# Optimization experiments

Hardware: AMD Instinct MI355X
Metric: run time of the kernel (lower is better)

Reference implementation:

```python
import jax, jax.numpy as jnp
import numpy as np

B, S, D = 4, 4096, 64


def setup_inputs() -> dict:
    key = jax.random.key(0)
    ks = jax.random.split(key, 11)
    std = 1.0 / np.sqrt(D)
    inp = {
        "q": jax.random.normal(ks[0], (B, S, D), jnp.float32),
        "k": jax.random.normal(ks[1], (B, S, D), jnp.float32),
        "v": jax.random.normal(ks[2], (B, S, D), jnp.float32),
        # torch.nn.Linear params: weight [out,in], bias [out]
        "Wq": jax.random.uniform(ks[3], (D, D), jnp.float32, -std, std),
        "bq": jax.random.uniform(ks[4], (D,), jnp.float32, -std, std),
        "Wk": jax.random.uniform(ks[5], (D, D), jnp.float32, -std, std),
        "bk": jax.random.uniform(ks[6], (D,), jnp.float32, -std, std),
        "Wv": jax.random.uniform(ks[7], (D, D), jnp.float32, -std, std),
        "bv": jax.random.uniform(ks[8], (D,), jnp.float32, -std, std),
        "Wp": jax.random.uniform(ks[9], (D, D), jnp.float32, -std, std),
        "bp": jax.random.uniform(ks[10], (D,), jnp.float32, -std, std),
    }
    return inp


def reference(q, k, v, Wq, bq, Wk, bk, Wv, bv, Wp, bp):
    Q = q @ Wq.T + bq                      # [B,S,D]
    K = k @ Wk.T + bk
    V = v @ Wv.T + bv
    scale = 1.0 / jnp.sqrt(jnp.asarray(Q.shape[-1], Q.dtype))
    s = jnp.einsum('bqd,bkd->bqk', Q, K) * scale   # [B,S,S]
    # faithful to torch.tril(full_like(-inf), diagonal=-1): -inf strictly below diagonal
    i = jnp.arange(S)[:, None]
    j = jnp.arange(S)[None, :]
    s = jnp.where(i > j, -jnp.inf, s)
    o = jax.nn.softmax(s, axis=-1) @ V             # [B,S,D]
    return o @ Wp.T + bp
```

## Files before the change

### kernel.cpp

```cpp
#include <hip/hip_runtime.h>
#include <hip/hip_bf16.h>

#define S_LEN 4096
#define D_DIM 64
#define NBATCH 4

typedef unsigned short u16;
typedef unsigned int u32;
typedef __attribute__((ext_vector_type(8))) __bf16 bf16x8;
typedef __attribute__((ext_vector_type(4))) float f32x4;
typedef __attribute__((ext_vector_type(16))) float f32x16;

__device__ __forceinline__ u16 f_to_bf16u(float f) {
    union { float f; u32 u; } x; x.f = f;
    u32 r = x.u + 0x7fffu + ((x.u >> 16) & 1u);
    return (u16)(r >> 16);
}

__global__ __launch_bounds__(256, 2)
void proj_qkv_kernel(const float* __restrict__ q, const float* __restrict__ k,
                     const float* __restrict__ v,
                     const float* __restrict__ Wq, const float* __restrict__ bq,
                     const float* __restrict__ Wk, const float* __restrict__ bk,
                     const float* __restrict__ Wv, const float* __restrict__ bv,
                     u16* __restrict__ Qb, u16* __restrict__ Kb, u16* __restrict__ Vt)
{
    __shared__ __align__(16) u16 vt[64 * 72];

    const int p = blockIdx.y;
    const float* inp  = (p == 0) ? q  : (p == 1) ? k  : v;
    const float* W    = (p == 0) ? Wq : (p == 1) ? Wk : Wv;
    const float* bias = (p == 0) ? bq : (p == 1) ? bk : bv;
    const float scl   = (p == 0) ? 0.18033688011112042f : 1.0f;

    const int tid  = threadIdx.x;
    const int wid  = tid >> 6;
    const int lane = tid & 63;
    const int ln   = lane & 15;
    const int qd   = lane >> 4;
    const int row0 = blockIdx.x * 64;
    const int r0w  = row0 + wid * 16;

    bf16x8 afrag[2];
#pragma unroll
    for (int c = 0; c < 2; ++c) {
        const float* src = inp + (r0w + ln) * 64 + c * 32 + qd * 8;
        float4 f0 = *(const float4*)src;
        float4 f1 = *(const float4*)(src + 4);
        bf16x8 a;
        a[0] = (__bf16)f0.x; a[1] = (__bf16)f0.y; a[2] = (__bf16)f0.z; a[3] = (__bf16)f0.w;
        a[4] = (__bf16)f1.x; a[5] = (__bf16)f1.y; a[6] = (__bf16)f1.z; a[7] = (__bf16)f1.w;
        afrag[c] = a;
    }

    bf16x8 bfrag[4][2];
    float  bcol[4];
#pragma unroll
    for (int nb = 0; nb < 4; ++nb) {
        bcol[nb] = bias[nb * 16 + ln];
#pragma unroll
        for (int c = 0; c < 2; ++c) {
            const float* src = W + (nb * 16 + ln) * 64 + c * 32 + qd * 8;
            float4 f0 = *(const float4*)src;
            float4 f1 = *(const float4*)(src + 4);
            bf16x8 b;
            b[0] = (__bf16)f0.x; b[1] = (__bf16)f0.y; b[2] = (__bf16)f0.z; b[3] = (__bf16)f0.w;
            b[4] = (__bf16)f1.x; b[5] = (__bf16)f1.y; b[6] = (__bf16)f1.z; b[7] = (__bf16)f1.w;
            bfrag[nb][c] = b;
        }
    }

    f32x4 acc[4];
#pragma unroll
    for (int nb = 0; nb < 4; ++nb) acc[nb] = (f32x4){0.f, 0.f, 0.f, 0.f};
#pragma unroll
    for (int c = 0; c < 2; ++c)
#pragma unroll
        for (int nb = 0; nb < 4; ++nb)
            acc[nb] = __builtin_amdgcn_mfma_f32_16x16x32_bf16(afrag[c], bfrag[nb][c], acc[nb], 0, 0, 0);

    if (p < 2) {
        u16* dst = (p == 0) ? Qb : Kb;
#pragma unroll
        for (int nb = 0; nb < 4; ++nb)
#pragma unroll
            for (int r = 0; r < 4; ++r) {
                int row = r0w + qd * 4 + r;
                dst[row * 64 + nb * 16 + ln] = f_to_bf16u((acc[nb][r] + bcol[nb]) * scl);
            }
    } else {
#pragma unroll
        for (int nb = 0; nb < 4; ++nb)
#pragma unroll
            for (int r = 0; r < 4; ++r)
                vt[(wid * 16 + qd * 4 + r) * 72 + nb * 16 + ln] = f_to_bf16u(acc[nb][r] + bcol[nb]);
        __syncthreads();
        const int d  = tid >> 2;
        const int sc = tid & 3;
        const int b  = row0 >> 12;
        const int sb = row0 & 4095;
        __align__(16) u16 tmp[16];
#pragma unroll
        for (int i = 0; i < 16; ++i) tmp[i] = vt[(sc * 16 + i) * 72 + d];
        u16* dstp = Vt + (size_t)b * (64 * S_LEN) + d * S_LEN + sb + sc * 16;
        *(uint4*)(dstp)     = *(const uint4*)(tmp);
        *(uint4*)(dstp + 8) = *(const uint4*)(tmp + 8);
    }
}

__global__ __launch_bounds__(256, 2)
void flash_kernel(const u16* __restrict__ Qb, const u16* __restrict__ Kb,
                  const u16* __restrict__ Vt, u16* __restrict__ Op,
                  float* __restrict__ Lp)
{
    __shared__ __align__(16) u16 kv[2][2][64 * 64];
    __shared__ __align__(16) u16 pbuf[4][32 * 64];

    const int tid  = threadIdx.x;
    const int wid  = tid >> 6;
    const int lane = tid & 63;
    const int l31  = lane & 31;
    const int lh   = lane >> 5;
    const int sw7  = l31 & 7;

    const int bid   = blockIdx.x;
    const int half  = bid >> 8;
    const int idx   = bid & 255;
    const int batch = idx & 3;
    const int vv_   = idx >> 2;
    const int c     = vv_ & 3;
    const int rb16  = vv_ >> 2;
    const int rb    = half ? (31 - rb16) : rb16;
    const int first = 2 * rb;
    const int jt0   = first + ((c - first) & 3);
    const int i0w   = rb * 128 + wid * 32;

    const u16* qrow = Qb + ((size_t)batch * S_LEN + i0w + l31) * 64;
    bf16x8 qf[4];
#pragma unroll
    for (int c2 = 0; c2 < 4; ++c2)
        qf[c2] = *(const bf16x8*)(qrow + c2 * 16 + lh * 8);

    f32x16 o0, o1;
#pragma unroll
    for (int r = 0; r < 16; ++r) { o0[r] = 0.f; o1[r] = 0.f; }
    float lsum = 0.f;

    const int  srow = (tid & 127) >> 1;
    const int  sch0 = (tid & 1) * 4;
    const u16* kg   = Kb + ((size_t)batch * S_LEN + srow) * 64 + sch0 * 8;
    const u16* vg   = Vt + (size_t)batch * (64 * S_LEN) + srow * S_LEN + sch0 * 8;
    uint4 pf0, pf1, pf2, pf3;

    u16* pw = &pbuf[wid][0];
    int cur = 0;

    if (jt0 < 64) {
        {
            const int j0 = jt0 * 64;
            if (tid < 128) {
                const uint4* g = (const uint4*)(kg + (size_t)j0 * 64);
                pf0 = g[0]; pf1 = g[1]; pf2 = g[2]; pf3 = g[3];
            } else {
                const uint4* g = (const uint4*)(vg + j0);
                pf0 = g[0]; pf1 = g[1]; pf2 = g[2]; pf3 = g[3];
            }
            u16* base = &kv[0][(tid >> 7)][srow * 64];
            *(uint4*)(base + ((sch0 + 0) ^ (srow & 7)) * 8) = pf0;
            *(uint4*)(base + ((sch0 + 1) ^ (srow & 7)) * 8) = pf1;
            *(uint4*)(base + ((sch0 + 2) ^ (srow & 7)) * 8) = pf2;
            *(uint4*)(base + ((sch0 + 3) ^ (srow & 7)) * 8) = pf3;
        }

        for (int jt = jt0; jt < 64; jt += 4) {
            __syncthreads();
            const int j0   = jt * 64;
            const bool more = (jt + 4) < 64;
            if (more) {
                const int jn = (jt + 4) * 64;
                if (tid < 128) {
                    const uint4* g = (const uint4*)(kg + (size_t)jn * 64);
                    pf0 = g[0]; pf1 = g[1]; pf2 = g[2]; pf3 = g[3];
                } else {
                    const uint4* g = (const uint4*)(vg + jn);
                    pf0 = g[0]; pf1 = g[1]; pf2 = g[2]; pf3 = g[3];
                }
            }

            const u16* kb = &kv[cur][0][0];
            const u16* vb = &kv[cur][1][0];

            f32x16 s0, s1;
#pragma unroll
            for (int r = 0; r < 16; ++r) { s0[r] = 0.f; s1[r] = 0.f; }
#pragma unroll
            for (int c2 = 0; c2 < 4; ++c2) {
                const int ch = (2 * c2 + lh) ^ sw7;
                bf16x8 k0 = *(const bf16x8*)(kb + l31 * 64 + ch * 8);
                bf16x8 k1 = *(const bf16x8*)(kb + (32 + l31) * 64 + ch * 8);
                s0 = __builtin_amdgcn_mfma_f32_32x32x16_bf16(k0, qf[c2], s0, 0, 0, 0);
                s1 = __builtin_amdgcn_mfma_f32_32x32x16_bf16(k1, qf[c2], s1, 0, 0, 0);
            }

            const bool needmask = (j0 < i0w + 32);
            const int  qr = i0w + l31;
#pragma unroll
            for (int m = 0; m < 2; ++m) {
#pragma unroll
                for (int g = 0; g < 4; ++g) {
                    float p0, p1, p2, p3;
                    {
                        const f32x16& s = m ? s1 : s0;
                        p0 = exp2f(s[g * 4 + 0]);
                        p1 = exp2f(s[g * 4 + 1]);
                        p2 = exp2f(s[g * 4 + 2]);
                        p3 = exp2f(s[g * 4 + 3]);
                    }
                    if (needmask) {
                        const int kcol = j0 + m * 32 + 8 * g + 4 * lh;
                        p0 = (kcol + 0 < qr) ? 0.f : p0;
                        p1 = (kcol + 1 < qr) ? 0.f : p1;
                        p2 = (kcol + 2 < qr) ? 0.f : p2;
                        p3 = (kcol + 3 < qr) ? 0.f : p3;
                    }
                    lsum += (p0 + p1) + (p2 + p3);
                    u32 w0 = (u32)f_to_bf16u(p0) | ((u32)f_to_bf16u(p1) << 16);
                    u32 w1 = (u32)f_to_bf16u(p2) | ((u32)f_to_bf16u(p3) << 16);
                    *(uint2*)(pw + l31 * 64 + m * 32 + g * 8 + 4 * lh) = make_uint2(w0, w1);
                }
            }

#pragma unroll
            for (int cc = 0; cc < 4; ++cc) {
                bf16x8 pa = *(const bf16x8*)(pw + l31 * 64 + cc * 16 + lh * 8);
                const int ch = (2 * cc + lh) ^ sw7;
                bf16x8 va = *(const bf16x8*)(vb + l31 * 64 + ch * 8);
                bf16x8 vbq = *(const bf16x8*)(vb + (32 + l31) * 64 + ch * 8);
                o0 = __builtin_amdgcn_mfma_f32_32x32x16_bf16(pa, va, o0, 0, 0, 0);
                o1 = __builtin_amdgcn_mfma_f32_32x32x16_bf16(pa, vbq, o1, 0, 0, 0);
            }

            if (more) {
                u16* base = &kv[cur ^ 1][(tid >> 7)][srow * 64];
                *(uint4*)(base + ((sch0 + 0) ^ (srow & 7)) * 8) = pf0;
                *(uint4*)(base + ((sch0 + 1) ^ (srow & 7)) * 8) = pf1;
                *(uint4*)(base + ((sch0 + 2) ^ (srow & 7)) * 8) = pf2;
                *(uint4*)(base + ((sch0 + 3) ^ (srow & 7)) * 8) = pf3;
            }
            cur ^= 1;
        }
    }

    const int pt = ((batch * 32 + rb) * 4 + wid);
    u16* ob = Op + ((size_t)pt * 4 + c) * 2048;
#pragma unroll
    for (int r = 0; r < 16; ++r) {
        const int qrl = (r & 3) + 8 * (r >> 2) + 4 * lh;
        ob[qrl * 64 + l31]      = f_to_bf16u(o0[r]);
        ob[qrl * 64 + 32 + l31] = f_to_bf16u(o1[r]);
    }
    lsum += __shfl_xor(lsum, 32);
    if (lane < 32) Lp[((size_t)pt * 4 + c) * 32 + lane] = lsum;
}

__global__ __launch_bounds__(256, 2)
void combine_proj_kernel(const u16* __restrict__ Op, const float* __restrict__ Lp,
                         const float* __restrict__ Wp, const float* __restrict__ bp,
                         float* __restrict__ out)
{
    const int tid  = threadIdx.x;
    const int wid  = tid >> 6;
    const int lane = tid & 63;
    const int ln   = lane & 15;
    const int qd   = lane >> 4;
    const int g    = blockIdx.x * 64 + wid * 16;
    const int row  = g + ln;

    const int batch = row >> 12;
    const int sr    = row & 4095;
    const int pt    = (batch * 32 + (sr >> 7)) * 4 + ((sr >> 5) & 3);
    const int rl    = sr & 31;

    float acc0[8], acc1[8];
#pragma unroll
    for (int j = 0; j < 8; ++j) { acc0[j] = 0.f; acc1[j] = 0.f; }
    float l = 0.f;
#pragma unroll
    for (int cc = 0; cc < 4; ++cc) {
        const u16* op = Op + ((size_t)pt * 4 + cc) * 2048 + rl * 64 + qd * 8;
        bf16x8 x0 = *(const bf16x8*)op;
        bf16x8 x1 = *(const bf16x8*)(op + 32);
#pragma unroll
        for (int j = 0; j < 8; ++j) { acc0[j] += (float)x0[j]; acc1[j] += (float)x1[j]; }
        l += Lp[((size_t)pt * 4 + cc) * 32 + rl];
    }
    float inv = 1.0f / l;
    bf16x8 afrag[2];
#pragma unroll
    for (int j = 0; j < 8; ++j) { afrag[0][j] = (__bf16)(acc0[j] * inv); afrag[1][j] = (__bf16)(acc1[j] * inv); }

    bf16x8 bfrag[4][2];
    float  bcol[4];
#pragma unroll
    for (int nb = 0; nb < 4; ++nb) {
        bcol[nb] = bp[nb * 16 + ln];
#pragma unroll
        for (int cc = 0; cc < 2; ++cc) {
            const float* src = Wp + (nb * 16 + ln) * 64 + cc * 32 + qd * 8;
            float4 f0 = *(const float4*)src;
            float4 f1 = *(const float4*)(src + 4);
            bf16x8 b;
            b[0] = (__bf16)f0.x; b[1] = (__bf16)f0.y; b[2] = (__bf16)f0.z; b[3] = (__bf16)f0.w;
            b[4] = (__bf16)f1.x; b[5] = (__bf16)f1.y; b[6] = (__bf16)f1.z; b[7] = (__bf16)f1.w;
            bfrag[nb][cc] = b;
        }
    }

    f32x4 acc[4];
#pragma unroll
    for (int nb = 0; nb < 4; ++nb) acc[nb] = (f32x4){0.f, 0.f, 0.f, 0.f};
#pragma unroll
    for (int cc = 0; cc < 2; ++cc)
#pragma unroll
        for (int nb = 0; nb < 4; ++nb)
            acc[nb] = __builtin_amdgcn_mfma_f32_16x16x32_bf16(afrag[cc], bfrag[nb][cc], acc[nb], 0, 0, 0);

#pragma unroll
    for (int nb = 0; nb < 4; ++nb)
#pragma unroll
        for (int r = 0; r < 4; ++r) {
            int rowo = g + qd * 4 + r;
            out[(size_t)rowo * 64 + nb * 16 + ln] = acc[nb][r] + bcol[nb];
        }
}

extern "C" void kernel_launch(void* const* d_in, const int* in_sizes, int n_in,
                              void* d_out, int out_size, void* d_ws, size_t ws_size,
                              hipStream_t stream) {
    const float* q  = (const float*)d_in[0];
    const float* k  = (const float*)d_in[1];
    const float* v  = (const float*)d_in[2];
    const float* Wq = (const float*)d_in[3];
    const float* bq = (const float*)d_in[4];
    const float* Wk = (const float*)d_in[5];
    const float* bk = (const float*)d_in[6];
    const float* Wv = (const float*)d_in[7];
    const float* bv = (const float*)d_in[8];
    const float* Wp = (const float*)d_in[9];
    const float* bp = (const float*)d_in[10];
    float* out = (float*)d_out;

    const size_t NTOK = (size_t)NBATCH * S_LEN * D_DIM;
    u16* Qb = (u16*)d_ws;
    u16* Kb = Qb + NTOK;
    u16* Vt = Kb + NTOK;
    u16* Op = Vt + NTOK;
    float* Lp = (float*)(Op + (size_t)4096 * 1024);

    proj_qkv_kernel<<<dim3(256, 3), 256, 0, stream>>>(q, k, v, Wq, bq, Wk, bk, Wv, bv, Qb, Kb, Vt);
    flash_kernel<<<512, 256, 0, stream>>>(Qb, Kb, Vt, Op, Lp);
    combine_proj_kernel<<<256, 256, 0, stream>>>(Op, Lp, Wp, bp, out);
}
```

Measured before the change: 129.7 us.

## Enlarge flash tiles to 128x128 with 2x2 wave split and paired bands

Restructures the flash kernel so each block processes a 128-query by 128-key tile, with the four waves split 2x2 over query and key halves. Each block handles two complementary bands (p and 31-p) for load balance, so half as many blocks are launched, and dynamic LDS (100KB) holds larger double-buffered K/V tiles. Partial outputs now come in 8 slots per band (4 key phases × 2 key halves), which the combine kernel sums. The aim is more reuse of each K/V load and fewer barriers per unit of work, at the cost of occupancy dropping to one block per CU and extra partial-output traffic.

```diff
diff --git a/kernel.cpp b/kernel.cpp
--- a/kernel.cpp
+++ b/kernel.cpp
@@ -108,159 +108,182 @@
     }
 }
 
-__global__ __launch_bounds__(256, 2)
+__global__ __launch_bounds__(256, 1)
 void flash_kernel(const u16* __restrict__ Qb, const u16* __restrict__ Kb,
                   const u16* __restrict__ Vt, u16* __restrict__ Op,
                   float* __restrict__ Lp)
 {
-    __shared__ __align__(16) u16 kv[2][2][64 * 64];
-    __shared__ __align__(16) u16 pbuf[4][32 * 64];
-
-    const int tid  = threadIdx.x;
-    const int wid  = tid >> 6;
-    const int lane = tid & 63;
-    const int l31  = lane & 31;
-    const int lh   = lane >> 5;
-    const int sw7  = l31 & 7;
+    extern __shared__ __align__(16) u16 dynlds[];
+    u16* kvbuf = dynlds;
+    u16* pbuf  = dynlds + 32768;
+
+    const int tid   = threadIdx.x;
+    const int wid   = tid >> 6;
+    const int lane  = tid & 63;
+    const int l31   = lane & 31;
+    const int lh    = lane >> 5;
+    const int qhalf = wid & 1;
+    const int khalf = wid >> 1;
 
     const int bid   = blockIdx.x;
-    const int half  = bid >> 8;
-    const int idx   = bid & 255;
-    const int batch = idx & 3;
-    const int vv_   = idx >> 2;
-    const int c     = vv_ & 3;
-    const int rb16  = vv_ >> 2;
-    const int rb    = half ? (31 - rb16) : rb16;
-    const int first = 2 * rb;
-    const int jt0   = first + ((c - first) & 3);
-    const int i0w   = rb * 128 + wid * 32;
-
-    const u16* qrow = Qb + ((size_t)batch * S_LEN + i0w + l31) * 64;
-    bf16x8 qf[4];
-#pragma unroll
-    for (int c2 = 0; c2 < 4; ++c2)
-        qf[c2] = *(const bf16x8*)(qrow + c2 * 16 + lh * 8);
-
-    f32x16 o0, o1;
-#pragma unroll
-    for (int r = 0; r < 16; ++r) { o0[r] = 0.f; o1[r] = 0.f; }
-    float lsum = 0.f;
-
-    const int  srow = (tid & 127) >> 1;
+    const int batch = bid & 3;
+    const int c     = (bid >> 2) & 3;
+    const int p     = bid >> 4;
+
+    const int  srow = tid >> 1;
     const int  sch0 = (tid & 1) * 4;
-    const u16* kg   = Kb + ((size_t)batch * S_LEN + srow) * 64 + sch0 * 8;
-    const u16* vg   = Vt + (size_t)batch * (64 * S_LEN) + srow * S_LEN + sch0 * 8;
-    uint4 pf0, pf1, pf2, pf3;
-
-    u16* pw = &pbuf[wid][0];
+    const int  vrow = tid >> 2;
+    const int  vch0 = (tid & 3) * 4;
+    const u16* kgp  = Kb + ((size_t)batch * S_LEN + srow) * 64;
+    const u16* vgp  = Vt + (size_t)batch * (64 * S_LEN) + (size_t)vrow * S_LEN;
+
+    u16* pw = pbuf + wid * (64 * 72);
     int cur = 0;
 
-    if (jt0 < 64) {
+    for (int ph = 0; ph < 2; ++ph) {
+        const int band = ph ? (31 - p) : p;
+        const int jt0  = band + ((c - band) & 3);
+
+        bf16x8 qf[2][4];
         {
-            const int j0 = jt0 * 64;
-            if (tid < 128) {
-                const uint4* g = (const uint4*)(kg + (size_t)j0 * 64);
-                pf0 = g[0]; pf1 = g[1]; pf2 = g[2]; pf3 = g[3];
-            } else {
-                const uint4* g = (const uint4*)(vg + j0);
-                pf0 = g[0]; pf1 = g[1]; pf2 = g[2]; pf3 = g[3];
+            const u16* qb = Qb + ((size_t)batch * S_LEN + band * 128 + qhalf * 64 + l31) * 64;
+#pragma unroll
+            for (int ni = 0; ni < 2; ++ni)
+#pragma unroll
+                for (int c2 = 0; c2 < 4; ++c2)
+                    qf[ni][c2] = *(const bf16x8*)(qb + ni * (32 * 64) + c2 * 16 + lh * 8);
+        }
+
+        f32x16 o00, o01, o10, o11;
+#pragma unroll
+        for (int r = 0; r < 16; ++r) { o00[r] = 0.f; o01[r] = 0.f; o10[r] = 0.f; o11[r] = 0.f; }
+        float ls0 = 0.f, ls1 = 0.f;
+
+        if (jt0 < 32) {
+            {
+                const int j0 = jt0 * 128;
+                const uint4* gk = (const uint4*)(kgp + (size_t)j0 * 64);
+                u16* kb = kvbuf + cur * 16384 + srow * 64;
+#pragma unroll
+                for (int i = 0; i < 4; ++i)
+                    *(uint4*)(kb + ((sch0 + i) ^ (srow & 7)) * 8) = gk[sch0 + i];
+                const uint4* gv = (const uint4*)(vgp + j0);
+                u16* vb = kvbuf + cur * 16384 + 8192 + vrow * 128;
+#pragma unroll
+                for (int i = 0; i < 4; ++i) {
+                    const int chv = vch0 + i;
+                    *(uint4*)(vb + ((chv & 8) | ((chv ^ vrow) & 7)) * 8) = gv[chv];
+                }
             }
-            u16* base = &kv[0][(tid >> 7)][srow * 64];
-            *(uint4*)(base + ((sch0 + 0) ^ (srow & 7)) * 8) = pf0;
-            *(uint4*)(base + ((sch0 + 1) ^ (srow & 7)) * 8) = pf1;
-            *(uint4*)(base + ((sch0 + 2) ^ (srow & 7)) * 8) = pf2;
-            *(uint4*)(base + ((sch0 + 3) ^ (srow & 7)) * 8) = pf3;
-        }
-
-        for (int jt = jt0; jt < 64; jt += 4) {
-            __syncthreads();
-            const int j0   = jt * 64;
-            const bool more = (jt + 4) < 64;
-            if (more) {
-                const int jn = (jt + 4) * 64;
-                if (tid < 128) {
-                    const uint4* g = (const uint4*)(kg + (size_t)jn * 64);
-                    pf0 = g[0]; pf1 = g[1]; pf2 = g[2]; pf3 = g[3];
-                } else {
-                    const uint4* g = (const uint4*)(vg + jn);
-                    pf0 = g[0]; pf1 = g[1]; pf2 = g[2]; pf3 = g[3];
-                }
+
+            for (int jt = jt0; jt < 32; jt += 4) {
+                __syncthreads();
+                const bool more = (jt + 4) < 32;
+                uint4 kpf[4], vpf[4];
+                if (more) {
+                    const int jn = (jt + 4) * 128;
+                    const uint4* gk = (const uint4*)(kgp + (size_t)jn * 64);
+#pragma unroll
+                    for (int i = 0; i < 4; ++i) kpf[i] = gk[sch0 + i];
+                    const uint4* gv = (const uint4*)(vgp + jn);
+#pragma unroll
+                    for (int i = 0; i < 4; ++i) vpf[i] = gv[vch0 + i];
+                }
+                const u16* kb = kvbuf + cur * 16384;
+                const u16* vb = kvbuf + cur * 16384 + 8192;
+                const bool dm = (jt == band);
+
+#pragma unroll
+                for (int mi = 0; mi < 2; ++mi) {
+                    f32x16 s0, s1;
+#pragma unroll
+                    for (int r = 0; r < 16; ++r) { s0[r] = 0.f; s1[r] = 0.f; }
+                    const int rK = khalf * 64 + mi * 32 + l31;
+#pragma unroll
+                    for (int c2 = 0; c2 < 4; ++c2) {
+                        bf16x8 a = *(const bf16x8*)(kb + rK * 64 + (((2 * c2 + lh) ^ (rK & 7)) * 8));
+                        s0 = __builtin_amdgcn_mfma_f32_32x32x16_bf16(a, qf[0][c2], s0, 0, 0, 0);
+                        s1 = __builtin_amdgcn_mfma_f32_32x32x16_bf16(a, qf[1][c2], s1, 0, 0, 0);
+                    }
+#pragma unroll
+                    for (int ni = 0; ni < 2; ++ni) {
+                        float lacc = 0.f;
+#pragma unroll
+                        for (int g = 0; g < 4; ++g) {
+                            float p0, p1, p2, p3;
+                            {
+                                const f32x16& s = ni ? s1 : s0;
+                                p0 = exp2f(s[g * 4 + 0]);
+                                p1 = exp2f(s[g * 4 + 1]);
+                                p2 = exp2f(s[g * 4 + 2]);
+                                p3 = exp2f(s[g * 4 + 3]);
+                            }
+                            if (dm) {
+                                const int kg = khalf * 64 + mi * 32 + 8 * g + 4 * lh;
+                                const int qg = qhalf * 64 + ni * 32 + l31;
+                                p0 = (kg + 0 < qg) ? 0.f : p0;
+                                p1 = (kg + 1 < qg) ? 0.f : p1;
+                                p2 = (kg + 2 < qg) ? 0.f : p2;
+                                p3 = (kg + 3 < qg) ? 0.f : p3;
+                            }
+                            lacc += (p0 + p1) + (p2 + p3);
+                            u32 w0 = (u32)f_to_bf16u(p0) | ((u32)f_to_bf16u(p1) << 16);
+                            u32 w1 = (u32)f_to_bf16u(p2) | ((u32)f_to_bf16u(p3) << 16);
+                            *(uint2*)(pw + (ni * 32 + l31) * 72 + mi * 32 + g * 8 + 4 * lh) = make_uint2(w0, w1);
+                        }
+                        if (ni) ls1 += lacc; else ls0 += lacc;
+                    }
+                }
+
+#pragma unroll
+                for (int c2 = 0; c2 < 4; ++c2) {
+                    bf16x8 pa0 = *(const bf16x8*)(pw + l31 * 72 + c2 * 16 + lh * 8);
+                    bf16x8 pa1 = *(const bf16x8*)(pw + (32 + l31) * 72 + c2 * 16 + lh * 8);
+                    const int chv = khalf * 8 + c2 * 2 + lh;
+                    const int r0 = l31, r1 = 32 + l31;
+                    bf16x8 v0 = *(const bf16x8*)(vb + r0 * 128 + (((chv & 8) | ((chv ^ (r0 & 7)) & 7)) * 8));
+                    bf16x8 v1 = *(const bf16x8*)(vb + r1 * 128 + (((chv & 8) | ((chv ^ (r1 & 7)) & 7)) * 8));
+                    o00 = __builtin_amdgcn_mfma_f32_32x32x16_bf16(pa0, v0, o00, 0, 0, 0);
+                    o01 = __builtin_amdgcn_mfma_f32_32x32x16_bf16(pa0, v1, o01, 0, 0, 0);
+                    o10 = __builtin_amdgcn_mfma_f32_32x32x16_bf16(pa1, v0, o10, 0, 0, 0);
+                    o11 = __builtin_amdgcn_mfma_f32_32x32x16_bf16(pa1, v1, o11, 0, 0, 0);
+                }
+
+                if (more) {
+                    u16* kb2 = kvbuf + (cur ^ 1) * 16384 + srow * 64;
+#pragma unroll
+                    for (int i = 0; i < 4; ++i)
+                        *(uint4*)(kb2 + ((sch0 + i) ^ (srow & 7)) * 8) = kpf[i];
+                    u16* vb2 = kvbuf + (cur ^ 1) * 16384 + 8192 + vrow * 128;
+#pragma unroll
+                    for (int i = 0; i < 4; ++i) {
+                        const int chv = vch0 + i;
+                        *(uint4*)(vb2 + ((chv & 8) | ((chv ^ vrow) & 7)) * 8) = vpf[i];
+                    }
+                }
+                cur ^= 1;
             }
-
-            const u16* kb = &kv[cur][0][0];
-            const u16* vb = &kv[cur][1][0];
-
-            f32x16 s0, s1;
-#pragma unroll
-            for (int r = 0; r < 16; ++r) { s0[r] = 0.f; s1[r] = 0.f; }
-#pragma unroll
-            for (int c2 = 0; c2 < 4; ++c2) {
-                const int ch = (2 * c2 + lh) ^ sw7;
-                bf16x8 k0 = *(const bf16x8*)(kb + l31 * 64 + ch * 8);
-                bf16x8 k1 = *(const bf16x8*)(kb + (32 + l31) * 64 + ch * 8);
-                s0 = __builtin_amdgcn_mfma_f32_32x32x16_bf16(k0, qf[c2], s0, 0, 0, 0);
-                s1 = __builtin_amdgcn_mfma_f32_32x32x16_bf16(k1, qf[c2], s1, 0, 0, 0);
-            }
-
-            const bool needmask = (j0 < i0w + 32);
-            const int  qr = i0w + l31;
-#pragma unroll
-            for (int m = 0; m < 2; ++m) {
-#pragma unroll
-                for (int g = 0; g < 4; ++g) {
-                    float p0, p1, p2, p3;
-                    {
-                        const f32x16& s = m ? s1 : s0;
-                        p0 = exp2f(s[g * 4 + 0]);
-                        p1 = exp2f(s[g * 4 + 1]);
-                        p2 = exp2f(s[g * 4 + 2]);
-                        p3 = exp2f(s[g * 4 + 3]);
-                    }
-                    if (needmask) {
-                        const int kcol = j0 + m * 32 + 8 * g + 4 * lh;
-                        p0 = (kcol + 0 < qr) ? 0.f : p0;
-                        p1 = (kcol + 1 < qr) ? 0.f : p1;
-                        p2 = (kcol + 2 < qr) ? 0.f : p2;
-                        p3 = (kcol + 3 < qr) ? 0.f : p3;
-                    }
-                    lsum += (p0 + p1) + (p2 + p3);
-                    u32 w0 = (u32)f_to_bf16u(p0) | ((u32)f_to_bf16u(p1) << 16);
-                    u32 w1 = (u32)f_to_bf16u(p2) | ((u32)f_to_bf16u(p3) << 16);
-                    *(uint2*)(pw + l31 * 64 + m * 32 + g * 8 + 4 * lh) = make_uint2(w0, w1);
-                }
-            }
-
-#pragma unroll
-            for (int cc = 0; cc < 4; ++cc) {
-                bf16x8 pa = *(const bf16x8*)(pw + l31 * 64 + cc * 16 + lh * 8);
-                const int ch = (2 * cc + lh) ^ sw7;
-                bf16x8 va = *(const bf16x8*)(vb + l31 * 64 + ch * 8);
-                bf16x8 vbq = *(const bf16x8*)(vb + (32 + l31) * 64 + ch * 8);
-                o0 = __builtin_amdgcn_mfma_f32_32x32x16_bf16(pa, va, o0, 0, 0, 0);
-                o1 = __builtin_amdgcn_mfma_f32_32x32x16_bf16(pa, vbq, o1, 0, 0, 0);
-            }
-
-            if (more) {
-                u16* base = &kv[cur ^ 1][(tid >> 7)][srow * 64];
-                *(uint4*)(base + ((sch0 + 0) ^ (srow & 7)) * 8) = pf0;
-                *(uint4*)(base + ((sch0 + 1) ^ (srow & 7)) * 8) = pf1;
-                *(uint4*)(base + ((sch0 + 2) ^ (srow & 7)) * 8) = pf2;
-                *(uint4*)(base + ((sch0 + 3) ^ (srow & 7)) * 8) = pf3;
-            }
-            cur ^= 1;
-        }
-    }
-
-    const int pt = ((batch * 32 + rb) * 4 + wid);
-    u16* ob = Op + ((size_t)pt * 4 + c) * 2048;
-#pragma unroll
-    for (int r = 0; r < 16; ++r) {
-        const int qrl = (r & 3) + 8 * (r >> 2) + 4 * lh;
-        ob[qrl * 64 + l31]      = f_to_bf16u(o0[r]);
-        ob[qrl * 64 + 32 + l31] = f_to_bf16u(o1[r]);
-    }
-    lsum += __shfl_xor(lsum, 32);
-    if (lane < 32) Lp[((size_t)pt * 4 + c) * 32 + lane] = lsum;
+        }
+
+        const int slot = ((batch * 32 + band) * 4 + c) * 2 + khalf;
+        u16* ob = Op + (size_t)slot * 8192;
+#pragma unroll
+        for (int r = 0; r < 16; ++r) {
+            const int rowf = (r & 3) + 8 * (r >> 2) + 4 * lh;
+            const int r0   = (qhalf * 64 + rowf) * 64;
+            const int r1   = (qhalf * 64 + 32 + rowf) * 64;
+            ob[r0 + l31]      = f_to_bf16u(o00[r]);
+            ob[r0 + 32 + l31] = f_to_bf16u(o01[r]);
+            ob[r1 + l31]      = f_to_bf16u(o10[r]);
+            ob[r1 + 32 + l31] = f_to_bf16u(o11[r]);
+        }
+        ls0 += __shfl_xor(ls0, 32);
+        ls1 += __shfl_xor(ls1, 32);
+        if (lh == 0) {
+            Lp[slot * 128 + qhalf * 64 + l31]      = ls0;
+            Lp[slot * 128 + qhalf * 64 + 32 + l31] = ls1;
+        }
+    }
 }
 
 __global__ __launch_bounds__(256, 2)
@@ -278,21 +301,23 @@
 
     const int batch = row >> 12;
     const int sr    = row & 4095;
-    const int pt    = (batch * 32 + (sr >> 7)) * 4 + ((sr >> 5) & 3);
-    const int rl    = sr & 31;
+    const int band  = sr >> 7;
+    const int rl    = sr & 127;
+    const int sbase = ((batch * 32 + band) * 4) * 2;
 
     float acc0[8], acc1[8];
 #pragma unroll
     for (int j = 0; j < 8; ++j) { acc0[j] = 0.f; acc1[j] = 0.f; }
     float l = 0.f;
 #pragma unroll
-    for (int cc = 0; cc < 4; ++cc) {
-        const u16* op = Op + ((size_t)pt * 4 + cc) * 2048 + rl * 64 + qd * 8;
+    for (int s = 0; s < 8; ++s) {
+        const int slot = sbase + s;
+        const u16* op = Op + (size_t)slot * 8192 + rl * 64 + qd * 8;
         bf16x8 x0 = *(const bf16x8*)op;
         bf16x8 x1 = *(const bf16x8*)(op + 32);
 #pragma unroll
         for (int j = 0; j < 8; ++j) { acc0[j] += (float)x0[j]; acc1[j] += (float)x1[j]; }
-        l += Lp[((size_t)pt * 4 + cc) * 32 + rl];
+        l += Lp[slot * 128 + rl];
     }
     float inv = 1.0f / l;
     bf16x8 afrag[2];
@@ -355,9 +380,16 @@
     u16* Kb = Qb + NTOK;
     u16* Vt = Kb + NTOK;
     u16* Op = Vt + NTOK;
-    float* Lp = (float*)(Op + (size_t)4096 * 1024);
+    float* Lp = (float*)(Op + (size_t)1024 * 8192);
+
+    static bool attr_set = false;
+    if (!attr_set) {
+        hipFuncSetAttribute((const void*)flash_kernel,
+                            hipFuncAttributeMaxDynamicSharedMemorySize, 102400);
+        attr_set = true;
+    }
 
     proj_qkv_kernel<<<dim3(256, 3), 256, 0, stream>>>(q, k, v, Wq, bq, Wk, bk, Wv, bv, Qb, Kb, Vt);
-    flash_kernel<<<512, 256, 0, stream>>>(Qb, Kb, Vt, Op, Lp);
+    flash_kernel<<<256, 256, 102400, stream>>>(Qb, Kb, Vt, Op, Lp);
     combine_proj_kernel<<<256, 256, 0, stream>>>(Op, Lp, Wp, bp, out);
 }
```

Measured after the change: 146.5 us. 1.13x slower.

## Rebalance flash work: pair causal bands per block, split KV eight ways

Applied to the files above, without the earlier changes.

Each flash block now handles two paired query bands (band p and 31-p) in sequence, and the KV range is split into 8 interleaved chunks instead of 4. This keeps the causal workload even across blocks. The shared-memory layout drops the XOR swizzle in favour of a padded row stride of 66 elements, every thread loads both K and V, and bf16 packing uses the HIP intrinsic. The combine kernel now sums eight partial outputs per row, which adds partial-output traffic and more reduction work. The padded stride leaves 16-byte LDS accesses misaligned, which may cost performance or correctness.

```diff
diff --git a/kernel.cpp b/kernel.cpp
--- a/kernel.cpp
+++ b/kernel.cpp
@@ -15,6 +15,12 @@
     union { float f; u32 u; } x; x.f = f;
     u32 r = x.u + 0x7fffu + ((x.u >> 16) & 1u);
     return (u16)(r >> 16);
+}
+
+__device__ __forceinline__ u32 pack_bf16_2(float a, float b) {
+    union { __hip_bfloat162 h; u32 u; } z;
+    z.h = __float22bfloat162_rn(float2{a, b});
+    return z.u;
 }
 
 __global__ __launch_bounds__(256, 2)
@@ -108,159 +114,156 @@
     }
 }
 
+#define KSTR 66
+#define KTILE (64 * KSTR)
+
 __global__ __launch_bounds__(256, 2)
 void flash_kernel(const u16* __restrict__ Qb, const u16* __restrict__ Kb,
                   const u16* __restrict__ Vt, u16* __restrict__ Op,
                   float* __restrict__ Lp)
 {
-    __shared__ __align__(16) u16 kv[2][2][64 * 64];
-    __shared__ __align__(16) u16 pbuf[4][32 * 64];
+    __shared__ __align__(16) u16 kv[2][2 * KTILE];
+    __shared__ __align__(16) u16 pbuf[4][32 * KSTR];
 
     const int tid  = threadIdx.x;
     const int wid  = tid >> 6;
     const int lane = tid & 63;
     const int l31  = lane & 31;
     const int lh   = lane >> 5;
-    const int sw7  = l31 & 7;
 
     const int bid   = blockIdx.x;
-    const int half  = bid >> 8;
-    const int idx   = bid & 255;
-    const int batch = idx & 3;
-    const int vv_   = idx >> 2;
-    const int c     = vv_ & 3;
-    const int rb16  = vv_ >> 2;
-    const int rb    = half ? (31 - rb16) : rb16;
-    const int first = 2 * rb;
-    const int jt0   = first + ((c - first) & 3);
-    const int i0w   = rb * 128 + wid * 32;
-
-    const u16* qrow = Qb + ((size_t)batch * S_LEN + i0w + l31) * 64;
-    bf16x8 qf[4];
-#pragma unroll
-    for (int c2 = 0; c2 < 4; ++c2)
-        qf[c2] = *(const bf16x8*)(qrow + c2 * 16 + lh * 8);
-
-    f32x16 o0, o1;
-#pragma unroll
-    for (int r = 0; r < 16; ++r) { o0[r] = 0.f; o1[r] = 0.f; }
-    float lsum = 0.f;
-
-    const int  srow = (tid & 127) >> 1;
-    const int  sch0 = (tid & 1) * 4;
-    const u16* kg   = Kb + ((size_t)batch * S_LEN + srow) * 64 + sch0 * 8;
-    const u16* vg   = Vt + (size_t)batch * (64 * S_LEN) + srow * S_LEN + sch0 * 8;
-    uint4 pf0, pf1, pf2, pf3;
+    const int batch = bid & 3;
+    const int c     = (bid >> 2) & 7;
+    const int p     = bid >> 5;
+
+    const int  srow = tid >> 2;
+    const int  sch0 = (tid & 3) * 2;
+    const u16* kgp  = Kb + ((size_t)batch * S_LEN + srow) * 64 + sch0 * 8;
+    const u16* vgp  = Vt + (size_t)batch * (64 * S_LEN) + (size_t)srow * S_LEN + sch0 * 8;
 
     u16* pw = &pbuf[wid][0];
     int cur = 0;
 
-    if (jt0 < 64) {
+    for (int ph = 0; ph < 2; ++ph) {
+        const int band = ph ? (31 - p) : p;
+        const int i0w  = band * 128 + wid * 32;
+        const int jt0  = 2 * band + ((c - 2 * band) & 7);
+
+        bf16x8 qf[4];
         {
-            const int j0 = jt0 * 64;
-            if (tid < 128) {
-                const uint4* g = (const uint4*)(kg + (size_t)j0 * 64);
-                pf0 = g[0]; pf1 = g[1]; pf2 = g[2]; pf3 = g[3];
-            } else {
-                const uint4* g = (const uint4*)(vg + j0);
-                pf0 = g[0]; pf1 = g[1]; pf2 = g[2]; pf3 = g[3];
+            const u16* qb = Qb + ((size_t)batch * S_LEN + i0w + l31) * 64;
+#pragma unroll
+            for (int c2 = 0; c2 < 4; ++c2)
+                qf[c2] = *(const bf16x8*)(qb + c2 * 16 + lh * 8);
+        }
+
+        f32x16 o0, o1;
+#pragma unroll
+        for (int r = 0; r < 16; ++r) { o0[r] = 0.f; o1[r] = 0.f; }
+        float lsum = 0.f;
+
+        if (jt0 < 64) {
+            __syncthreads();
+            {
+                const int j0 = jt0 * 64;
+                uint4 k0 = *(const uint4*)(kgp + (size_t)j0 * 64);
+                uint4 k1 = *(const uint4*)(kgp + (size_t)j0 * 64 + 8);
+                uint4 v0 = *(const uint4*)(vgp + j0);
+                uint4 v1 = *(const uint4*)(vgp + j0 + 8);
+                u16* kb = &kv[cur][srow * KSTR];
+                *(uint4*)(kb + (sch0 + 0) * 8) = k0;
+                *(uint4*)(kb + (sch0 + 1) * 8) = k1;
+                u16* vb = &kv[cur][KTILE + srow * KSTR];
+                *(uint4*)(vb + (sch0 + 0) * 8) = v0;
+                *(uint4*)(vb + (sch0 + 1) * 8) = v1;
             }
-            u16* base = &kv[0][(tid >> 7)][srow * 64];
-            *(uint4*)(base + ((sch0 + 0) ^ (srow & 7)) * 8) = pf0;
-            *(uint4*)(base + ((sch0 + 1) ^ (srow & 7)) * 8) = pf1;
-            *(uint4*)(base + ((sch0 + 2) ^ (srow & 7)) * 8) = pf2;
-            *(uint4*)(base + ((sch0 + 3) ^ (srow & 7)) * 8) = pf3;
-        }
-
-        for (int jt = jt0; jt < 64; jt += 4) {
-            __syncthreads();
-            const int j0   = jt * 64;
-            const bool more = (jt + 4) < 64;
-            if (more) {
-                const int jn = (jt + 4) * 64;
-                if (tid < 128) {
-                    const uint4* g = (const uint4*)(kg + (size_t)jn * 64);
-                    pf0 = g[0]; pf1 = g[1]; pf2 = g[2]; pf3 = g[3];
-                } else {
-                    const uint4* g = (const uint4*)(vg + jn);
-                    pf0 = g[0]; pf1 = g[1]; pf2 = g[2]; pf3 = g[3];
-                }
+
+            for (int jt = jt0; jt < 64; jt += 8) {
+                __syncthreads();
+                const bool more = (jt + 8) < 64;
+                uint4 kp0, kp1, vp0, vp1;
+                if (more) {
+                    const int jn = (jt + 8) * 64;
+                    kp0 = *(const uint4*)(kgp + (size_t)jn * 64);
+                    kp1 = *(const uint4*)(kgp + (size_t)jn * 64 + 8);
+                    vp0 = *(const uint4*)(vgp + jn);
+                    vp1 = *(const uint4*)(vgp + jn + 8);
+                }
+                const u16* kb = &kv[cur][0];
+                const u16* vb = &kv[cur][KTILE];
+                const int j0 = jt * 64;
+                const bool needmask = (j0 < i0w + 32);
+                const int qr = i0w + l31 - j0;
+
+                f32x16 s0, s1;
+#pragma unroll
+                for (int r = 0; r < 16; ++r) { s0[r] = 0.f; s1[r] = 0.f; }
+#pragma unroll
+                for (int c2 = 0; c2 < 4; ++c2) {
+                    bf16x8 a0 = *(const bf16x8*)(kb + l31 * KSTR + c2 * 16 + lh * 8);
+                    bf16x8 a1 = *(const bf16x8*)(kb + (32 + l31) * KSTR + c2 * 16 + lh * 8);
+                    s0 = __builtin_amdgcn_mfma_f32_32x32x16_bf16(a0, qf[c2], s0, 0, 0, 0);
+                    s1 = __builtin_amdgcn_mfma_f32_32x32x16_bf16(a1, qf[c2], s1, 0, 0, 0);
+                }
+
+#pragma unroll
+                for (int mi = 0; mi < 2; ++mi) {
+#pragma unroll
+                    for (int g = 0; g < 4; ++g) {
+                        float p0, p1, p2, p3;
+                        {
+                            const f32x16& s = mi ? s1 : s0;
+                            p0 = exp2f(s[g * 4 + 0]);
+                            p1 = exp2f(s[g * 4 + 1]);
+                            p2 = exp2f(s[g * 4 + 2]);
+                            p3 = exp2f(s[g * 4 + 3]);
+                        }
+                        if (needmask) {
+                            const int kg = mi * 32 + g * 8 + 4 * lh;
+                            p0 = (kg + 0 < qr) ? 0.f : p0;
+                            p1 = (kg + 1 < qr) ? 0.f : p1;
+                            p2 = (kg + 2 < qr) ? 0.f : p2;
+                            p3 = (kg + 3 < qr) ? 0.f : p3;
+                        }
+                        lsum += (p0 + p1) + (p2 + p3);
+                        u32 w0 = pack_bf16_2(p0, p1);
+                        u32 w1 = pack_bf16_2(p2, p3);
+                        *(uint2*)(pw + l31 * KSTR + mi * 32 + g * 8 + 4 * lh) = make_uint2(w0, w1);
+                    }
+                }
+
+#pragma unroll
+                for (int c2 = 0; c2 < 4; ++c2) {
+                    bf16x8 pa = *(const bf16x8*)(pw + l31 * KSTR + c2 * 16 + lh * 8);
+                    bf16x8 v0 = *(const bf16x8*)(vb + l31 * KSTR + c2 * 16 + lh * 8);
+                    bf16x8 v1 = *(const bf16x8*)(vb + (32 + l31) * KSTR + c2 * 16 + lh * 8);
+                    o0 = __builtin_amdgcn_mfma_f32_32x32x16_bf16(pa, v0, o0, 0, 0, 0);
+                    o1 = __builtin_amdgcn_mfma_f32_32x32x16_bf16(pa, v1, o1, 0, 0, 0);
+                }
+
+                if (more) {
+                    u16* kb2 = &kv[cur ^ 1][srow * KSTR];
+                    *(uint4*)(kb2 + (sch0 + 0) * 8) = kp0;
+                    *(uint4*)(kb2 + (sch0 + 1) * 8) = kp1;
+                    u16* vb2 = &kv[cur ^ 1][KTILE + srow * KSTR];
+                    *(uint4*)(vb2 + (sch0 + 0) * 8) = vp0;
+                    *(uint4*)(vb2 + (sch0 + 1) * 8) = vp1;
+                }
+                cur ^= 1;
             }
-
-            const u16* kb = &kv[cur][0][0];
-            const u16* vb = &kv[cur][1][0];
-
-            f32x16 s0, s1;
-#pragma unroll
-            for (int r = 0; r < 16; ++r) { s0[r] = 0.f; s1[r] = 0.f; }
-#pragma unroll
-            for (int c2 = 0; c2 < 4; ++c2) {
-                const int ch = (2 * c2 + lh) ^ sw7;
-                bf16x8 k0 = *(const bf16x8*)(kb + l31 * 64 + ch * 8);
-                bf16x8 k1 = *(const bf16x8*)(kb + (32 + l31) * 64 + ch * 8);
-                s0 = __builtin_amdgcn_mfma_f32_32x32x16_bf16(k0, qf[c2], s0, 0, 0, 0);
-                s1 = __builtin_amdgcn_mfma_f32_32x32x16_bf16(k1, qf[c2], s1, 0, 0, 0);
-            }
-
-            const bool needmask = (j0 < i0w + 32);
-            const int  qr = i0w + l31;
-#pragma unroll
-            for (int m = 0; m < 2; ++m) {
-#pragma unroll
-                for (int g = 0; g < 4; ++g) {
-                    float p0, p1, p2, p3;
-                    {
-                        const f32x16& s = m ? s1 : s0;
-                        p0 = exp2f(s[g * 4 + 0]);
-                        p1 = exp2f(s[g * 4 + 1]);
-                        p2 = exp2f(s[g * 4 + 2]);
-                        p3 = exp2f(s[g * 4 + 3]);
-                    }
-                    if (needmask) {
-                        const int kcol = j0 + m * 32 + 8 * g + 4 * lh;
-                        p0 = (kcol + 0 < qr) ? 0.f : p0;
-                        p1 = (kcol + 1 < qr) ? 0.f : p1;
-                        p2 = (kcol + 2 < qr) ? 0.f : p2;
-                        p3 = (kcol + 3 < qr) ? 0.f : p3;
-                    }
-                    lsum += (p0 + p1) + (p2 + p3);
-                    u32 w0 = (u32)f_to_bf16u(p0) | ((u32)f_to_bf16u(p1) << 16);
-                    u32 w1 = (u32)f_to_bf16u(p2) | ((u32)f_to_bf16u(p3) << 16);
-                    *(uint2*)(pw + l31 * 64 + m * 32 + g * 8 + 4 * lh) = make_uint2(w0, w1);
-                }
-            }
-
-#pragma unroll
-            for (int cc = 0; cc < 4; ++cc) {
-                bf16x8 pa = *(const bf16x8*)(pw + l31 * 64 + cc * 16 + lh * 8);
-                const int ch = (2 * cc + lh) ^ sw7;
-                bf16x8 va = *(const bf16x8*)(vb + l31 * 64 + ch * 8);
-                bf16x8 vbq = *(const bf16x8*)(vb + (32 + l31) * 64 + ch * 8);
-                o0 = __builtin_amdgcn_mfma_f32_32x32x16_bf16(pa, va, o0, 0, 0, 0);
-                o1 = __builtin_amdgcn_mfma_f32_32x32x16_bf16(pa, vbq, o1, 0, 0, 0);
-            }
-
-            if (more) {
-                u16* base = &kv[cur ^ 1][(tid >> 7)][srow * 64];
-                *(uint4*)(base + ((sch0 + 0) ^ (srow & 7)) * 8) = pf0;
-                *(uint4*)(base + ((sch0 + 1) ^ (srow & 7)) * 8) = pf1;
-                *(uint4*)(base + ((sch0 + 2) ^ (srow & 7)) * 8) = pf2;
-                *(uint4*)(base + ((sch0 + 3) ^ (srow & 7)) * 8) = pf3;
-            }
-            cur ^= 1;
-        }
-    }
-
-    const int pt = ((batch * 32 + rb) * 4 + wid);
-    u16* ob = Op + ((size_t)pt * 4 + c) * 2048;
-#pragma unroll
-    for (int r = 0; r < 16; ++r) {
-        const int qrl = (r & 3) + 8 * (r >> 2) + 4 * lh;
-        ob[qrl * 64 + l31]      = f_to_bf16u(o0[r]);
-        ob[qrl * 64 + 32 + l31] = f_to_bf16u(o1[r]);
-    }
-    lsum += __shfl_xor(lsum, 32);
-    if (lane < 32) Lp[((size_t)pt * 4 + c) * 32 + lane] = lsum;
+        }
+
+        const int slot = (batch * 32 + band) * 8 + c;
+        u16* ob = Op + (size_t)slot * 8192;
+#pragma unroll
+        for (int r = 0; r < 16; ++r) {
+            const int qrl = (r & 3) + 8 * (r >> 2) + 4 * lh;
+            ob[(wid * 32 + qrl) * 64 + l31]      = f_to_bf16u(o0[r]);
+            ob[(wid * 32 + qrl) * 64 + 32 + l31] = f_to_bf16u(o1[r]);
+        }
+        lsum += __shfl_xor(lsum, 32);
+        if (lh == 0) Lp[slot * 128 + wid * 32 + l31] = lsum;
+    }
 }
 
 __global__ __launch_bounds__(256, 2)
@@ -278,21 +281,23 @@
 
     const int batch = row >> 12;
     const int sr    = row & 4095;
-    const int pt    = (batch * 32 + (sr >> 7)) * 4 + ((sr >> 5) & 3);
-    const int rl    = sr & 31;
+    const int band  = sr >> 7;
+    const int rl    = sr & 127;
+    const int sbase = (batch * 32 + band) * 8;
 
     float acc0[8], acc1[8];
 #pragma unroll
     for (int j = 0; j < 8; ++j) { acc0[j] = 0.f; acc1[j] = 0.f; }
     float l = 0.f;
 #pragma unroll
-    for (int cc = 0; cc < 4; ++cc) {
-        const u16* op = Op + ((size_t)pt * 4 + cc) * 2048 + rl * 64 + qd * 8;
+    for (int s = 0; s < 8; ++s) {
+        const int slot = sbase + s;
+        const u16* op = Op + (size_t)slot * 8192 + rl * 64 + qd * 8;
         bf16x8 x0 = *(const bf16x8*)op;
         bf16x8 x1 = *(const bf16x8*)(op + 32);
 #pragma unroll
         for (int j = 0; j < 8; ++j) { acc0[j] += (float)x0[j]; acc1[j] += (float)x1[j]; }
-        l += Lp[((size_t)pt * 4 + cc) * 32 + rl];
+        l += Lp[slot * 128 + rl];
     }
     float inv = 1.0f / l;
     bf16x8 afrag[2];
@@ -355,7 +360,7 @@
     u16* Kb = Qb + NTOK;
     u16* Vt = Kb + NTOK;
     u16* Op = Vt + NTOK;
-    float* Lp = (float*)(Op + (size_t)4096 * 1024);
+    float* Lp = (float*)(Op + (size_t)1024 * 8192);
 
     proj_qkv_kernel<<<dim3(256, 3), 256, 0, stream>>>(q, k, v, Wq, bq, Wk, bk, Wv, bv, Qb, Kb, Vt);
     flash_kernel<<<512, 256, 0, stream>>>(Qb, Kb, Vt, Op, Lp);
```

Result: slower. 165.1 us (+27.2%).
